# Optimization experiments

Hardware: AMD Instinct MI355X
Metric: run time of the kernel (lower is better)

## Reference

```python
import jax, jax.numpy as jnp
import numpy as np
from jax import lax

C = 128; HEADS = 16; HD = 8; EPS = 1e-5

def _conv3x3(x, w):
    return lax.conv_general_dilated(x, w, (1, 1), 'SAME', dimension_numbers=('NCHW', 'OIHW', 'NCHW'))

def _cbr3(x, w, g, b):
    # Conv3x3 + BatchNorm(eval, running stats folded -> per-channel affine) + ReLU
    return jax.nn.relu(_conv3x3(x, w) * g[:, None, None] + b[:, None, None])

def _cbr1(x, w, g, b):
    y = jnp.einsum('bchw,oc->bohw', x, w)
    return jax.nn.relu(y * g[:, None, None] + b[:, None, None])

def _ln(t, g, b):
    mu = t.mean(-1, keepdims=True)
    va = ((t - mu) ** 2).mean(-1, keepdims=True)
    return (t - mu) / jnp.sqrt(va + EPS) * g + b

def _gconv1x1(xf, w, b, groups):
    # grouped 1x1 conv on flattened spatial dim: xf [B,Cin,N], w [Cout, Cin//groups]
    B, Cin, N = xf.shape
    Cout = w.shape[0]
    y = jnp.einsum('bgcn,goc->bgon', xf.reshape(B, groups, Cin // groups, N),
                   w.reshape(groups, Cout // groups, Cin // groups))
    return y.reshape(B, Cout, N) + b[:, None]

def _ss_softmax(a):
    # sign * sqrt(|a| + 1e-5) then softmax (GISSA's custom transform)
    a = jnp.sign(a) * jnp.sqrt(jnp.abs(a) + 1e-5)
    return jax.nn.softmax(a, axis=-1)

def _gissa(ximg, qkv_w, qkv_b, g, b, qkv2_w, qkv2_b):
    B, Cc, H, W = ximg.shape
    N = H * W
    xf = ximg.reshape(B, Cc, N)
    qkv = _gconv1x1(xf, qkv_w, qkv_b, HEADS).reshape(B, 3, HEADS, HD, N)
    q, k, v = qkv[:, 0], qkv[:, 1], qkv[:, 2]
    attn = _ss_softmax(jnp.einsum('bhdn,bhen->bhde', q, k) * HD ** -0.5)  # [B,h,hd,hd]
    x1 = jnp.einsum('bhde,bhen->bhdn', attn, v).reshape(B, Cc, N) + xf
    x1 = x1.reshape(B, HEADS, HD, N).transpose(0, 2, 1, 3).reshape(B, Cc, N)  # channel shuffle
    y = x1 * g[:, None] + b[:, None]  # BatchNorm eval affine
    xr = jax.nn.relu(y)
    qkv2 = _gconv1x1(xr, qkv2_w, qkv2_b, HD).reshape(B, 3, HD, HEADS, N)
    q2, k2, v2 = qkv2[:, 0], qkv2[:, 1], qkv2[:, 2]
    attn2 = _ss_softmax(jnp.einsum('bdhn,bdgn->bdhg', q2, k2) * HEADS ** -0.5)  # [B,hd,h,h]
    o = jnp.einsum('bdhg,bdgn->bdhn', attn2, v2).transpose(0, 2, 1, 3).reshape(B, Cc, N) + y
    return o.reshape(B, Cc, H, W)

def _swsa_calc(ximg, pi_w, pi_b, g, b, po_w, po_b):
    B, Cc, H, W = ximg.shape
    t = jnp.einsum('bcn,oc->bon', ximg.reshape(B, Cc, H * W), pi_w) + pi_b[:, None]
    t = t * g[:, None] + b[:, None]  # BN affine
    q = t[:, :Cc].transpose(0, 2, 1)  # [B,N,C]
    v = t[:, Cc:].transpose(0, 2, 1)
    atn = jax.nn.softmax(jnp.einsum('bnc,bmc->bnm', q, q) * Cc ** -0.5, axis=-1)
    y = jnp.einsum('bnm,bmc->bnc', atn, v).transpose(0, 2, 1)  # [B,C,N]
    y = (jnp.einsum('bcn,oc->bon', y, po_w) + po_b[:, None]).reshape(B, Cc, H, W)
    return y, atn

def _swsa_reuse(ximg, atn, pi_w, pi_b, g, b, po_w, po_b):
    B, Cc, H, W = ximg.shape
    t = jnp.einsum('bcn,oc->bon', ximg.reshape(B, Cc, H * W), pi_w) + pi_b[:, None]
    t = t * g[:, None] + b[:, None]
    v = t.transpose(0, 2, 1)
    y = (jnp.einsum('bnm,bmc->bnc', atn, v) * Cc ** -0.5).transpose(0, 2, 1)
    return (jnp.einsum('bcn,oc->bon', y, po_w) + po_b[:, None]).reshape(B, Cc, H, W)

def _forward(x, ssfe_w, ssfe_g, ssfe_b, cc_w, cc_g, cc_b, ln1_g, ln1_b, qkv_w, qkv_b, gbn_g, gbn_b, qkv2_w, qkv2_b, ln2_g, ln2_b, mlp_w1, mlp_b1, mlp_w2, mlp_b2, cs_w, cs_g, cs_b, lfe0_w, lfe0_g, lfe0_b, s0_pi_w, s0_pi_b, s0_bn_g, s0_bn_b, s0_po_w, s0_po_b, lfe1_w, lfe1_g, lfe1_b, s1_pi_w, s1_pi_b, s1_bn_g, s1_bn_b, s1_po_w, s1_po_b, lamuda, fc_w):
    B, Cin, H, W = x.shape
    N = H * W
    # SSFE stem (approximated as Conv3x3+BN+ReLU; source def unavailable)
    xs = _cbr3(x, ssfe_w, ssfe_g, ssfe_b)
    # channel branch: 1x1 CBR + SIT (LN -> GISSA -> residual -> LN -> MLP -> residual)
    xc = _cbr1(xs, cc_w, cc_g, cc_b)
    t = xc.reshape(B, C, N).transpose(0, 2, 1)  # [B,N,C]
    cur = _ln(t, ln1_g, ln1_b).transpose(0, 2, 1).reshape(B, C, H, W)
    t = t + _gissa(cur, qkv_w, qkv_b, gbn_g, gbn_b, qkv2_w, qkv2_b).reshape(B, C, N).transpose(0, 2, 1)
    h = _ln(t, ln2_g, ln2_b)
    h = jax.nn.gelu(h @ mlp_w1.T + mlp_b1, approximate=False) @ mlp_w2.T + mlp_b2
    t = t + h
    xc = t.transpose(0, 2, 1).reshape(B, C, H, W)
    # spatial branch: 3x3 CBR + SCA (LFE + SWSA with attention reuse)
    xp = _cbr3(xs, cs_w, cs_g, cs_b)
    xp = _cbr3(xp, lfe0_w, lfe0_g, lfe0_b) + xp
    y, atn = _swsa_calc(xp, s0_pi_w, s0_pi_b, s0_bn_g, s0_bn_b, s0_po_w, s0_po_b)
    xp = y + xp
    xp = _cbr3(xp, lfe1_w, lfe1_g, lfe1_b) + xp
    xp = _swsa_reuse(xp, atn, s1_pi_w, s1_pi_b, s1_bn_g, s1_bn_b, s1_po_w, s1_po_b) + xp
    lmd = jax.nn.sigmoid(lamuda[0])
    out = lmd * xc + (1.0 - lmd) * xp
    return out.mean(axis=(2, 3)) @ fc_w.T  # global avg pool + fc (dropout p=0 for HUST2013)

def setup_inputs():
    ks = iter(jax.random.split(jax.random.key(0), 64))
    def rn(shape, scale=0.05):
        return jax.random.normal(next(ks), shape, jnp.float32) * scale
    ones = lambda *s: jnp.ones(s, jnp.float32)
    zeros = lambda *s: jnp.zeros(s, jnp.float32)
    return dict(
        x=jax.random.normal(next(ks), (32, 144, 32, 32), jnp.float32),
        ssfe_w=rn((144, 144, 3, 3)), ssfe_g=ones(144), ssfe_b=zeros(144),
        cc_w=rn((128, 144)), cc_g=ones(128), cc_b=zeros(128),
        ln1_g=ones(128), ln1_b=zeros(128),
        qkv_w=rn((384, 8)), qkv_b=zeros(384),
        gbn_g=ones(128), gbn_b=zeros(128),
        qkv2_w=rn((384, 16)), qkv2_b=zeros(384),
        ln2_g=ones(128), ln2_b=zeros(128),
        mlp_w1=rn((512, 128)), mlp_b1=zeros(512),
        mlp_w2=rn((128, 512)), mlp_b2=zeros(128),
        cs_w=rn((128, 144, 3, 3)), cs_g=ones(128), cs_b=zeros(128),
        lfe0_w=rn((128, 128, 3, 3)), lfe0_g=ones(128), lfe0_b=zeros(128),
        s0_pi_w=rn((256, 128)), s0_pi_b=zeros(256), s0_bn_g=ones(256), s0_bn_b=zeros(256),
        s0_po_w=rn((128, 128)), s0_po_b=zeros(128),
        lfe1_w=rn((128, 128, 3, 3)), lfe1_g=ones(128), lfe1_b=zeros(128),
        s1_pi_w=rn((128, 128)), s1_pi_b=zeros(128), s1_bn_g=ones(128), s1_bn_b=zeros(128),
        s1_po_w=rn((128, 128)), s1_po_b=zeros(128),
        lamuda=jnp.full((1,), 0.5, jnp.float32),
        fc_w=rn((16, 128)),
    )

def reference(x, ssfe_w, ssfe_g, ssfe_b, cc_w, cc_g, cc_b, ln1_g, ln1_b, qkv_w, qkv_b, gbn_g, gbn_b, qkv2_w, qkv2_b, ln2_g, ln2_b, mlp_w1, mlp_b1, mlp_w2, mlp_b2, cs_w, cs_g, cs_b, lfe0_w, lfe0_g, lfe0_b, s0_pi_w, s0_pi_b, s0_bn_g, s0_bn_b, s0_po_w, s0_po_b, lfe1_w, lfe1_g, lfe1_b, s1_pi_w, s1_pi_b, s1_bn_g, s1_bn_b, s1_po_w, s1_po_b, lamuda, fc_w):
    return _forward(x, ssfe_w, ssfe_g, ssfe_b, cc_w, cc_g, cc_b, ln1_g, ln1_b, qkv_w, qkv_b, gbn_g, gbn_b, qkv2_w, qkv2_b, ln2_g, ln2_b, mlp_w1, mlp_b1, mlp_w2, mlp_b2, cs_w, cs_g, cs_b, lfe0_w, lfe0_g, lfe0_b, s0_pi_w, s0_pi_b, s0_bn_g, s0_bn_b, s0_po_w, s0_po_b, lfe1_w, lfe1_g, lfe1_b, s1_pi_w, s1_pi_b, s1_bn_g, s1_bn_b, s1_po_w, s1_po_b, lamuda, fc_w)
```

## Files before the change

kernel.cpp:

```cpp
#include <hip/hip_runtime.h>
#include <math.h>


static constexpr int NPIX = 1024;

typedef __attribute__((ext_vector_type(8))) short bf16x8;
typedef __attribute__((ext_vector_type(4))) float f32x4;
typedef __attribute__((ext_vector_type(8))) unsigned short u16x8;
typedef __attribute__((ext_vector_type(4))) unsigned short u16x4;

static __device__ __forceinline__ unsigned short f2bf(float f) {
    unsigned u = __builtin_bit_cast(unsigned, f);
    unsigned r = (u + 0x7fffu + ((u >> 16) & 1u)) >> 16;
    return (unsigned short)r;
}
static __device__ __forceinline__ float bf2f(unsigned short u) {
    unsigned v = ((unsigned)u) << 16;
    return __builtin_bit_cast(float, v);
}

__global__ __launch_bounds__(256) void prepack_convs(
    const float* __restrict__ ssfe_w, const float* __restrict__ cs_w,
    const float* __restrict__ lfe0_w, const float* __restrict__ lfe1_w,
    unsigned short* __restrict__ wssfe, unsigned short* __restrict__ wcs,
// ... 41 lines not shown
    } else if (idx < 102400) {
        v = po1_w[idx - 86016];
    } else if (idx < 167936) {
        v = w1[idx - 102400];
    } else {
        v = w2[idx - 167936];
    }
    o[idx] = f2bf(v);
}

__global__ __launch_bounds__(256) void cvt_xT_kernel(
    const float* __restrict__ x, unsigned short* __restrict__ xT0)
{
    __shared__ unsigned short T[64 * 168];
    const int tid = threadIdx.x;
    const int b = blockIdx.x;
    const int px0 = blockIdx.y << 6;
    const float* xb = x + ((size_t)b * 144 << 10) + px0;

#pragma unroll 1
    for (int idx = tid; idx < 72 * 64; idx += 256) {
        const int c2 = idx >> 6, px = idx & 63;
        float a = xb[((size_t)(2 * c2) << 10) + px];
        float c = xb[((size_t)(2 * c2 + 1) << 10) + px];
        *(unsigned*)&T[px * 168 + 2 * c2] =
            (unsigned)f2bf(a) | ((unsigned)f2bf(c) << 16);
    }
#pragma unroll 1
    for (int idx = tid; idx < 64 * 8; idx += 256) {
        const int px = idx >> 3, pr = idx & 7;
        *(unsigned*)&T[px * 168 + 144 + pr * 2] = 0u;
    }
    __syncthreads();

#pragma unroll 1
    for (int idx = tid; idx < 64 * 20; idx += 256) {
        const int px = idx / 20;
        const int chunk = idx - px * 20;
        *(u16x8*)(xT0 + ((size_t)((b << 10) + px0 + px)) * 160 + chunk * 8) =
            *(const u16x8*)&T[px * 168 + chunk * 8];
    }
}

__global__ __launch_bounds__(256) void conv3x3_ssfe_kernel(
    const unsigned short* __restrict__ xT,
    const unsigned short* __restrict__ wrep,
    const float* __restrict__ g, const float* __restrict__ bb,
    unsigned short* __restrict__ outT)
{
    constexpr int CINP = 160, PITCH = 168, NCHK = 20;
    __shared__ unsigned short X[130 * PITCH];
    const int tid = threadIdx.x;
    const int b = blockIdx.x, gr = blockIdx.y;
    const int pbase = gr << 6;
    const int gbase = pbase - 33;
    const int wid = tid >> 6, lane = tid & 63;
    const int ll = lane & 15, lq = lane >> 4;
    const unsigned short* xb = xT + ((size_t)b << 10) * CINP;

#pragma unroll 1
    for (int idx = tid; idx < 130 * NCHK; idx += 256) {
        const int row = idx / NCHK;
        const int chunk = idx - row * NCHK;
        const int gp = gbase + row;
        u16x8 v = {};
        if (gp >= 0 && gp < 1024)
            v = *(const u16x8*)(xb + (size_t)gp * CINP + chunk * 8);
        *(u16x8*)&X[row * PITCH + chunk * 8] = v;
    }
    __syncthreads();

    if (wid == 3) {
#pragma unroll
        for (int j = 0; j < 4; ++j) {
            const int px = pbase + j * 16 + ll;
            u16x4 z = {};
            *(u16x4*)(outT + ((size_t)((b << 10) + px)) * 160 + 144 + lq * 4) = z;
        }
        return;
    }

    const int co0w = wid * 48;
    f32x4 acc[3][4];
#pragma unroll
    for (int i = 0; i < 3; ++i)
#pragma unroll
        for (int j = 0; j < 4; ++j)
#pragma unroll
            for (int r = 0; r < 4; ++r) acc[i][j][r] = 0.f;

#pragma unroll
    for (int tap = 0; tap < 9; ++tap) {
        const int soff = (tap / 3) * 32 + (tap % 3);
        const int dx = tap % 3;
#pragma unroll
        for (int kc = 0; kc < CINP / 32; ++kc) {
            bf16x8 bfv[4];
#pragma unroll
            for (int j = 0; j < 4; ++j) {
                const int p = j * 16 + ll;
                bf16x8 v = *(const bf16x8*)&X[(p + soff) * PITCH + kc * 32 + lq * 8];
                const bool zed = (dx == 0 && (j & 1) == 0 && ll == 0) ||
                                 (dx == 2 && (j & 1) == 1 && ll == 15);
                if (zed) { bf16x8 z = {}; v = z; }
                bfv[j] = v;
            }
            const unsigned short* wb =
                wrep + ((size_t)tap * 144 + co0w) * CINP + kc * 32 + lq * 8;
#pragma unroll
            for (int i = 0; i < 3; ++i) {
                bf16x8 af = *(const bf16x8*)(wb + (size_t)(i * 16 + ll) * CINP);
#pragma unroll
                for (int j = 0; j < 4; ++j)
                    acc[i][j] = __builtin_amdgcn_mfma_f32_16x16x32_bf16(
                        af, bfv[j], acc[i][j], 0, 0, 0);
            }
        }
    }

#pragma unroll
    for (int i = 0; i < 3; ++i) {
        const int cob = co0w + i * 16 + lq * 4;
        float gv[4], bv[4];
#pragma unroll
        for (int r = 0; r < 4; ++r) { gv[r] = g[cob + r]; bv[r] = bb[cob + r]; }
#pragma unroll
        for (int j = 0; j < 4; ++j) {
            const int px = pbase + j * 16 + ll;
            u16x4 tp;
#pragma unroll
            for (int r = 0; r < 4; ++r)
                tp[r] = f2bf(fmaxf(acc[i][j][r] * gv[r] + bv[r], 0.f));
            *(u16x4*)(outT + ((size_t)((b << 10) + px)) * 160 + cob) = tp;
        }
    }
}

template <int CINP>
__global__ __launch_bounds__(256) void conv3x3_lds_kernel(
    const unsigned short* __restrict__ xT,
    const unsigned short* __restrict__ wrep,
    const float* __restrict__ g, const float* __restrict__ bb,
    const unsigned short* __restrict__ resT,
    unsigned short* __restrict__ outT, int Cout)
{
    constexpr int PITCH = CINP + 8;
    constexpr int NCHK = CINP / 8;
    __shared__ unsigned short X[130 * PITCH];
    const int tid = threadIdx.x;
    const int b = blockIdx.x, gr = blockIdx.y;
    const int pbase = gr << 6;
    const int gbase = pbase - 33;
    const int wid = tid >> 6, lane = tid & 63;
    const int ll = lane & 15, lq = lane >> 4;
    const int co0w = wid << 5;
    const unsigned short* xb = xT + ((size_t)b << 10) * CINP;

#pragma unroll 1
    for (int idx = tid; idx < 130 * NCHK; idx += 256) {
        const int row = idx / NCHK;
        const int chunk = idx - row * NCHK;
        const int gp = gbase + row;
        u16x8 v = {};
        if (gp >= 0 && gp < 1024)
            v = *(const u16x8*)(xb + (size_t)gp * CINP + chunk * 8);
        *(u16x8*)&X[row * PITCH + chunk * 8] = v;
    }
    __syncthreads();

    f32x4 acc[2][4];
#pragma unroll
    for (int i = 0; i < 2; ++i)
#pragma unroll
        for (int j = 0; j < 4; ++j)
#pragma unroll
            for (int r = 0; r < 4; ++r) acc[i][j][r] = 0.f;

#pragma unroll
    for (int tap = 0; tap < 9; ++tap) {
        const int soff = (tap / 3) * 32 + (tap % 3);
        const int dx = tap % 3;
#pragma unroll
        for (int kc = 0; kc < CINP / 32; ++kc) {
            bf16x8 bfv[4];
#pragma unroll
            for (int j = 0; j < 4; ++j) {
                const int p = j * 16 + ll;
                bf16x8 v = *(const bf16x8*)&X[(p + soff) * PITCH + kc * 32 + lq * 8];
                const bool zed = (dx == 0 && (j & 1) == 0 && ll == 0) ||
                                 (dx == 2 && (j & 1) == 1 && ll == 15);
                if (zed) { bf16x8 z = {}; v = z; }
                bfv[j] = v;
            }
            const unsigned short* wb =
                wrep + ((size_t)tap * Cout + co0w) * CINP + kc * 32 + lq * 8;
#pragma unroll
            for (int i = 0; i < 2; ++i) {
                bf16x8 af = *(const bf16x8*)(wb + (size_t)(i * 16 + ll) * CINP);
#pragma unroll
                for (int j = 0; j < 4; ++j)
                    acc[i][j] = __builtin_amdgcn_mfma_f32_16x16x32_bf16(
                        af, bfv[j], acc[i][j], 0, 0, 0);
            }
        }
    }

#pragma unroll
    for (int i = 0; i < 2; ++i) {
        const int cob = co0w + i * 16 + lq * 4;
        float gv[4], bv[4];
#pragma unroll
        for (int r = 0; r < 4; ++r) { gv[r] = g[cob + r]; bv[r] = bb[cob + r]; }
#pragma unroll
        for (int j = 0; j < 4; ++j) {
            const int px = pbase + j * 16 + ll;
            const size_t rowT = ((size_t)((b << 10) + px)) << 7;
            u16x4 rv = {};
            if (resT) rv = *(const u16x4*)(resT + rowT + cob);
            u16x4 tp;
#pragma unroll
            for (int r = 0; r < 4; ++r) {
                float v = fmaxf(acc[i][j][r] * gv[r] + bv[r], 0.f);
                if (resT) v += bf2f(rv[r]);
                tp[r] = f2bf(v);
            }
            *(u16x4*)(outT + rowT + cob) = tp;
        }
    }
}

template <int KP>
__global__ __launch_bounds__(256) void lin_mfma_kernel(
    const unsigned short* __restrict__ xT, const unsigned short* __restrict__ wbf,
    const float* __restrict__ bias0, const float* __restrict__ g,
    const float* __restrict__ bb, const unsigned short* __restrict__ resT,
    float* __restrict__ outF, unsigned short* __restrict__ outBF,
    unsigned short* __restrict__ outT, int do_relu)
{
    const int tid = threadIdx.x;
    const int b = blockIdx.x;
    const int n0 = blockIdx.y << 6;
    const int wid = tid >> 6, lane = tid & 63;
    const int ll = lane & 15, lq = lane >> 4;
    const unsigned short* xb = xT + (size_t)((b << 10) + n0) * KP;

    f32x4 acc[2][4];
#pragma unroll
    for (int i = 0; i < 2; ++i)
#pragma unroll
        for (int j = 0; j < 4; ++j)
#pragma unroll
            for (int r = 0; r < 4; ++r) acc[i][j][r] = 0.f;

#pragma unroll
    for (int kk = 0; kk < KP / 32; ++kk) {
        bf16x8 af[2], bfv[4];
#pragma unroll
        for (int i = 0; i < 2; ++i)
            af[i] = *(const bf16x8*)(wbf + (size_t)(wid * 32 + i * 16 + ll) * KP + kk * 32 + lq * 8);
#pragma unroll
        for (int j = 0; j < 4; ++j)
            bfv[j] = *(const bf16x8*)(xb + (size_t)(j * 16 + ll) * KP + kk * 32 + lq * 8);
#pragma unroll
        for (int i = 0; i < 2; ++i)
#pragma unroll
            for (int j = 0; j < 4; ++j)
                acc[i][j] = __builtin_amdgcn_mfma_f32_16x16x32_bf16(af[i], bfv[j], acc[i][j], 0, 0, 0);
    }

#pragma unroll
    for (int i = 0; i < 2; ++i) {
        const int cob = wid * 32 + i * 16 + lq * 4;
        float b0v[4], gv[4], bv[4];
#pragma unroll
        for (int r = 0; r < 4; ++r) {
            b0v[r] = bias0 ? bias0[cob + r] : 0.f;
            gv[r] = g ? g[cob + r] : 1.f;
            bv[r] = g ? bb[cob + r] : 0.f;
        }
#pragma unroll
        for (int j = 0; j < 4; ++j) {
            const int px = n0 + j * 16 + ll;
            const size_t rowT = ((size_t)((b << 10) + px)) << 7;
            u16x4 rv = {};
            if (resT) rv = *(const u16x4*)(resT + rowT + cob);
            u16x4 tp;
#pragma unroll
            for (int r = 0; r < 4; ++r) {
                const int co = cob + r;
                float v = acc[i][j][r] + b0v[r];
                v = v * gv[r] + bv[r];
                if (do_relu) v = fmaxf(v, 0.f);
                if (resT) v += bf2f(rv[r]);
                if (outF) outF[((size_t)((b << 7) + co) << 10) + px] = v;
                unsigned short h = f2bf(v);
                if (outBF) outBF[((size_t)((b << 7) + co) << 10) + px] = h;
                tp[r] = h;
            }
            if (outT) *(u16x4*)(outT + rowT + cob) = tp;
        }
    }
}

__global__ __launch_bounds__(256) void ln_kernel(
    const float* __restrict__ in, const float* __restrict__ g,
    const float* __restrict__ bb, unsigned short* __restrict__ out_bf,
    unsigned short* __restrict__ outT)
{
    const int tid = threadIdx.x;
    const int b = blockIdx.x >> 2;
    const int n = ((blockIdx.x & 3) << 8) + tid;
    const float* ib = in + ((size_t)b << 17) + n;
    float s = 0.f, sq = 0.f;
#pragma unroll 8
    for (int c = 0; c < 128; ++c) {
        float v = ib[(size_t)c << 10];
        s += v;
        sq += v * v;
    }
    const float mu = s * 0.0078125f;
    const float r = rsqrtf(sq * 0.0078125f - mu * mu + 1e-5f);
    unsigned short* obf = out_bf + ((size_t)b << 17) + n;
    unsigned short* oT = outT + (((size_t)b << 10) + n) * 128;
#pragma unroll 2
    for (int c0 = 0; c0 < 128; c0 += 8) {
        u16x8 pk;
#pragma unroll
        for (int e = 0; e < 8; ++e) {
            const int c = c0 + e;
            float v = ib[(size_t)c << 10];
            float y = (v - mu) * r * g[c] + bb[c];
            unsigned short h = f2bf(y);
            obf[(size_t)c << 10] = h;
            pk[e] = h;
        }
        *(u16x8*)(oT + c0) = pk;
    }
}

__global__ __launch_bounds__(256) void gram_kernel(
    const unsigned short* __restrict__ Xbf, float* __restrict__ G)
{
    __shared__ unsigned short Xs[128 * 128];
    const int tid = threadIdx.x;
    const int b = blockIdx.x >> 2;
    const int rg = blockIdx.x & 3;
    const int wid = tid >> 6, lane = tid & 63;
    const int lq = lane >> 4, ll = lane & 15;
    const unsigned short* Xb = Xbf + ((size_t)b << 17);

    f32x4 acc[2][2];
#pragma unroll
    for (int mi = 0; mi < 2; ++mi)
#pragma unroll
        for (int ci = 0; ci < 2; ++ci)
#pragma unroll
            for (int r = 0; r < 4; ++r) acc[mi][ci][r] = 0.f;

#pragma unroll 1
    for (int nt = 0; nt < 8; ++nt) {
        const int n0 = nt << 7;
#pragma unroll
        for (int p = 0; p < 8; ++p) {
            const int ch = (p << 4) + (tid >> 4);
            const int seg = (tid & 15) << 3;
            *(u16x8*)&Xs[ch * 128 + (seg ^ ((ch & 7) << 3))] =
                *(const u16x8*)(Xb + ((size_t)ch << 10) + n0 + seg);
        }
        __syncthreads();
#pragma unroll
        for (int ks = 0; ks < 4; ++ks) {
            bf16x8 af[2], bf_[2];
#pragma unroll
            for (int mi = 0; mi < 2; ++mi) {
                const int ar = (rg << 5) + mi * 16 + ll;
                af[mi] = *(const bf16x8*)&Xs[ar * 128 + ((ks * 32 + lq * 8) ^ ((ar & 7) << 3))];
            }
#pragma unroll
            for (int ci = 0; ci < 2; ++ci) {
                const int br = (wid << 5) + ci * 16 + ll;
                bf_[ci] = *(const bf16x8*)&Xs[br * 128 + ((ks * 32 + lq * 8) ^ ((br & 7) << 3))];
            }
#pragma unroll
            for (int mi = 0; mi < 2; ++mi)
#pragma unroll
                for (int ci = 0; ci < 2; ++ci)
                    acc[mi][ci] = __builtin_amdgcn_mfma_f32_16x16x32_bf16(
                        af[mi], bf_[ci], acc[mi][ci], 0, 0, 0);
        }
        __syncthreads();
    }
    float* Gb = G + ((size_t)b << 14);
#pragma unroll
    for (int mi = 0; mi < 2; ++mi)
#pragma unroll
        for (int ci = 0; ci < 2; ++ci)
#pragma unroll
            for (int r = 0; r < 4; ++r) {
                const int row = (rg << 5) + mi * 16 + lq * 4 + r;
                const int col = (wid << 5) + ci * 16 + ll;
                Gb[row * 128 + col] = acc[mi][ci][r];
            }
}

__global__ __launch_bounds__(256) void sums_kernel(
    const unsigned short* __restrict__ Xbf, float* __restrict__ S)
{
    const int tid = threadIdx.x;
    const int b = blockIdx.x;
    const int ch = tid >> 1, half = tid & 1;
    const unsigned short* p = Xbf + ((size_t)b << 17) + ((size_t)ch << 10) + half * 512;
    float s = 0.f;
#pragma unroll 4
    for (int i = 0; i < 64; ++i) {
        u16x8 v = *(const u16x8*)(p + i * 8);
#pragma unroll
        for (int e = 0; e < 8; ++e) s += bf2f(v[e]);
    }
    s += __shfl_xor(s, 1);
    if (half == 0) S[(b << 7) + ch] = s;
}

__global__ __launch_bounds__(64) void mats1_kernel(
    const float* __restrict__ G, const float* __restrict__ S,
    const float* __restrict__ qkv_w, const float* __restrict__ qkv_b,
    const float* __restrict__ g, const float* __restrict__ bb,
    unsigned short* __restrict__ M1, float* __restrict__ c1)
{
    const int lane = threadIdx.x;
    const int b = blockIdx.x >> 4, h = blockIdx.x & 15;
    const float* Gb = G + ((size_t)b << 14);
    const float* Sb = S + (b << 7);
    const int d = lane >> 3, e = lane & 7;
    const int qch = h * 8 + d, kch = 128 + h * 8 + e;
    const int qoff = (qch / 24) * 8, koff = (kch / 24) * 8;
    float wq[8], wk[8];
#pragma unroll
    for (int i = 0; i < 8; ++i) {
        wq[i] = qkv_w[qch * 8 + i];
        wk[i] = qkv_w[kch * 8 + i];
    }
    float s = 0.f;
#pragma unroll
    for (int i = 0; i < 8; ++i) {
        float gu = 0.f;
#pragma unroll
        for (int j = 0; j < 8; ++j) gu += Gb[(qoff + i) * 128 + koff + j] * wk[j];
        s += wq[i] * gu;
    }
    const float bq = qkv_b[qch], bk = qkv_b[kch];
    float swk = 0.f, swq = 0.f;
#pragma unroll
    for (int j = 0; j < 8; ++j) { swk += wk[j] * Sb[koff + j]; swq += wq[j] * Sb[qoff + j]; }
    s += bq * swk + bk * swq + 1024.f * bq * bk;
    s *= 0.35355339059327373f;
    float a = (s > 0.f) ? sqrtf(s + 1e-5f) : ((s < 0.f) ? -sqrtf(1e-5f - s) : 0.f);
    float mx = a;
    mx = fmaxf(mx, __shfl_xor(mx, 1));
    mx = fmaxf(mx, __shfl_xor(mx, 2));
    mx = fmaxf(mx, __shfl_xor(mx, 4));
    float p = __expf(a - mx);
    float den = p;
    den += __shfl_xor(den, 1);
    den += __shfl_xor(den, 2);
    den += __shfl_xor(den, 4);
    const float A = p / den;

    const int l = e;
    const int cp = d * 16 + h;
    float row[16];
#pragma unroll
    for (int j = 0; j < 16; ++j) row[j] = 0.f;
    float cacc = 0.f;
#pragma unroll
    for (int e2 = 0; e2 < 8; ++e2) {
        const float Ae = __shfl(A, d * 8 + e2);
        const int vch = 256 + h * 8 + e2;
        const int voff = (vch / 24) * 8;
        cacc += Ae * qkv_b[vch];
        if ((voff >> 4) == l) {
            const int base = voff & 15;
#pragma unroll
            for (int j = 0; j < 8; ++j) row[base + j] += Ae * qkv_w[vch * 8 + j];
        }
    }
    const int idc = h * 8 + d;
    if ((idc >> 4) == l) row[idc & 15] += 1.f;
    const float gg = g[cp];
    unsigned short* mrow = M1 + ((size_t)b << 14) + cp * 128 + l * 16;
#pragma unroll
    for (int j = 0; j < 16; ++j) mrow[j] = f2bf(gg * row[j]);
    if (l == 0) c1[(b << 7) + cp] = gg * cacc + bb[cp];
}

__global__ __launch_bounds__(256) void mats2_kernel(
    const float* __restrict__ G, const float* __restrict__ S,
    const float* __restrict__ qkv2_w, const float* __restrict__ qkv2_b,
    unsigned short* __restrict__ M2, float* __restrict__ c2)
{
    const int tid = threadIdx.x;
    const int b = blockIdx.x >> 3, d = blockIdx.x & 7;
    const float* Gb = G + ((size_t)b << 14);
    const float* Sb = S + (b << 7);
    const int h = tid >> 4, gq = tid & 15;
    const int q2ch = d * 16 + h, k2ch = 128 + d * 16 + gq;
    const int qoff = (q2ch / 48) * 16, koff = (k2ch / 48) * 16;
    float wq[16], wk[16];
#pragma unroll
    for (int i = 0; i < 16; ++i) {
        wq[i] = qkv2_w[q2ch * 16 + i];
        wk[i] = qkv2_w[k2ch * 16 + i];
    }
    float s = 0.f;
#pragma unroll
    for (int i = 0; i < 16; ++i) {
        float gu = 0.f;
#pragma unroll
        for (int j = 0; j < 16; ++j) gu += Gb[(qoff + i) * 128 + koff + j] * wk[j];
        s += wq[i] * gu;
    }
    const float bq = qkv2_b[q2ch], bk = qkv2_b[k2ch];
    float swk = 0.f, swq = 0.f;
#pragma unroll
    for (int j = 0; j < 16; ++j) { swk += wk[j] * Sb[koff + j]; swq += wq[j] * Sb[qoff + j]; }
    s += bq * swk + bk * swq + 1024.f * bq * bk;
    s *= 0.25f;
    float a = (s > 0.f) ? sqrtf(s + 1e-5f) : ((s < 0.f) ? -sqrtf(1e-5f - s) : 0.f);
    float mx = a;
    mx = fmaxf(mx, __shfl_xor(mx, 1));
    mx = fmaxf(mx, __shfl_xor(mx, 2));
    mx = fmaxf(mx, __shfl_xor(mx, 4));
    mx = fmaxf(mx, __shfl_xor(mx, 8));
    float p = __expf(a - mx);
    float den = p;
    den += __shfl_xor(den, 1);
    den += __shfl_xor(den, 2);
    den += __shfl_xor(den, 4);
    den += __shfl_xor(den, 8);
    const float A2 = p / den;

    const int l = gq;
    float row[8];
#pragma unroll
    for (int j = 0; j < 8; ++j) row[j] = 0.f;
    float cacc = 0.f;
#pragma unroll
    for (int g2 = 0; g2 < 16; ++g2) {
        const float Ag = __shfl(A2, (tid & 48) + g2);
        const int v2ch = 256 + d * 16 + g2;
        const int voff = (v2ch / 48) * 16;
        cacc += Ag * qkv2_b[v2ch];
        if ((l >> 1) == (voff >> 4)) {
            const int base = (l & 1) * 8;
#pragma unroll
            for (int j = 0; j < 8; ++j) row[j] += Ag * qkv2_w[v2ch * 16 + base + j];
        }
    }
    const int c = h * 8 + d;
    unsigned short* mrow = M2 + ((size_t)b << 14) + c * 128 + l * 8;
#pragma unroll
    for (int j = 0; j < 8; ++j) mrow[j] = f2bf(row[j]);
    if (l == 0) c2[(b << 7) + c] = cacc;
}

__global__ __launch_bounds__(256) void apply1_mfma_kernel(
    const unsigned short* __restrict__ curT, const unsigned short* __restrict__ M1bf,
    const float* __restrict__ c1, float* __restrict__ ybuf,
    unsigned short* __restrict__ yrbf, unsigned short* __restrict__ yrT)
{
    const int tid = threadIdx.x;
    const int b = blockIdx.x >> 3;
    const int n0 = (blockIdx.x & 7) << 7;
    const int wid = tid >> 6, lane = tid & 63;
    const int wr = wid >> 1, wc = wid & 1;
    const int ll = lane & 15, lq = lane >> 4;
    const unsigned short* Mb = M1bf + ((size_t)b << 14);
    const unsigned short* xb = curT + (((size_t)b << 10) + n0 + wc * 64) * 128;

    f32x4 acc[4][4];
#pragma unroll
    for (int i = 0; i < 4; ++i)
#pragma unroll
        for (int j = 0; j < 4; ++j)
#pragma unroll
            for (int r = 0; r < 4; ++r) acc[i][j][r] = 0.f;

#pragma unroll
    for (int kk = 0; kk < 4; ++kk) {
        bf16x8 af[4], bfv[4];
#pragma unroll
        for (int i = 0; i < 4; ++i)
            af[i] = *(const bf16x8*)(Mb + (size_t)(wr * 64 + i * 16 + ll) * 128 + kk * 32 + lq * 8);
#pragma unroll
        for (int j = 0; j < 4; ++j)
            bfv[j] = *(const bf16x8*)(xb + (size_t)(j * 16 + ll) * 128 + kk * 32 + lq * 8);
#pragma unroll
        for (int i = 0; i < 4; ++i)
#pragma unroll
            for (int j = 0; j < 4; ++j)
                acc[i][j] = __builtin_amdgcn_mfma_f32_16x16x32_bf16(af[i], bfv[j], acc[i][j], 0, 0, 0);
    }

#pragma unroll
    for (int i = 0; i < 4; ++i) {
        const int cob = wr * 64 + i * 16 + lq * 4;
        float c1v[4];
#pragma unroll
        for (int r = 0; r < 4; ++r) c1v[r] = c1[(b << 7) + cob + r];
#pragma unroll
        for (int j = 0; j < 4; ++j) {
            const int px = n0 + wc * 64 + j * 16 + ll;
            u16x4 tp;
#pragma unroll
            for (int r = 0; r < 4; ++r) {
                const int co = cob + r;
                const float v = acc[i][j][r] + c1v[r];
                const size_t oi = ((size_t)(b * 128 + co) << 10) + px;
                ybuf[oi] = v;
                const unsigned short h = f2bf(fmaxf(v, 0.f));
                yrbf[oi] = h;
                tp[r] = h;
            }
            *(u16x4*)(yrT + (((size_t)b << 10) + px) * 128 + cob) = tp;
        }
    }
}

__global__ __launch_bounds__(256) void apply2_mfma_kernel(
    const unsigned short* __restrict__ yrT, const unsigned short* __restrict__ M2bf,
    const float* __restrict__ c2, const float* __restrict__ ybuf,
    float* __restrict__ t)
{
    const int tid = threadIdx.x;
    const int b = blockIdx.x >> 3;
    const int n0 = (blockIdx.x & 7) << 7;
    const int wid = tid >> 6, lane = tid & 63;
    const int wr = wid >> 1, wc = wid & 1;
    const int ll = lane & 15, lq = lane >> 4;
    const unsigned short* Mb = M2bf + ((size_t)b << 14);
    const unsigned short* xb = yrT + (((size_t)b << 10) + n0 + wc * 64) * 128;

    f32x4 acc[4][4];
#pragma unroll
    for (int i = 0; i < 4; ++i)
#pragma unroll
        for (int j = 0; j < 4; ++j)
#pragma unroll
            for (int r = 0; r < 4; ++r) acc[i][j][r] = 0.f;

#pragma unroll
    for (int kk = 0; kk < 4; ++kk) {
        bf16x8 af[4], bfv[4];
#pragma unroll
        for (int i = 0; i < 4; ++i)
            af[i] = *(const bf16x8*)(Mb + (size_t)(wr * 64 + i * 16 + ll) * 128 + kk * 32 + lq * 8);
#pragma unroll
        for (int j = 0; j < 4; ++j)
            bfv[j] = *(const bf16x8*)(xb + (size_t)(j * 16 + ll) * 128 + kk * 32 + lq * 8);
#pragma unroll
        for (int i = 0; i < 4; ++i)
#pragma unroll
            for (int j = 0; j < 4; ++j)
                acc[i][j] = __builtin_amdgcn_mfma_f32_16x16x32_bf16(af[i], bfv[j], acc[i][j], 0, 0, 0);
    }

#pragma unroll
    for (int i = 0; i < 4; ++i) {
        const int cob = wr * 64 + i * 16 + lq * 4;
        float c2v[4];
#pragma unroll
        for (int r = 0; r < 4; ++r) c2v[r] = c2[(b << 7) + cob + r];
#pragma unroll
        for (int j = 0; j < 4; ++j) {
            const int px = n0 + wc * 64 + j * 16 + ll;
#pragma unroll
            for (int r = 0; r < 4; ++r) {
                const size_t oi = ((size_t)(b * 128 + cob + r) << 10) + px;
                t[oi] += acc[i][j][r] + c2v[r] + ybuf[oi];
            }
        }
    }
}

__global__ __launch_bounds__(256) void mlp_mfma_kernel(
    float* __restrict__ t, const float* __restrict__ ln_g,
    const float* __restrict__ ln_b, const unsigned short* __restrict__ w1bf,
    const float* __restrict__ b1, const unsigned short* __restrict__ w2bf,
    const float* __restrict__ b2)
{
    __shared__ unsigned char lds[16384 + 65536];
    unsigned char* xnb = lds;
    unsigned char* hb = lds + 16384;

    const int tid = threadIdx.x;
    const int b = blockIdx.x >> 4;
    const int n0 = (blockIdx.x & 15) << 6;
    float* tb = t + ((size_t)b << 17) + n0;

    {
        const int px = tid >> 2, q = tid & 3;
        float v[32];
        float s = 0.f, sq = 0.f;
#pragma unroll
        for (int k = 0; k < 32; ++k) {
            float x = tb[((size_t)(q * 32 + k) << 10) + px];
            v[k] = x;
            s += x;
            sq += x * x;
        }
        s += __shfl_xor(s, 1); s += __shfl_xor(s, 2);
        sq += __shfl_xor(sq, 1); sq += __shfl_xor(sq, 2);
        const float mu = s * 0.0078125f;
        const float rstd = rsqrtf(sq * 0.0078125f - mu * mu + 1e-5f);
        const int sw = (px & 7) << 4;
#pragma unroll
        for (int cc = 0; cc < 4; ++cc) {
            u16x8 pk;
#pragma unroll
            for (int e = 0; e < 8; ++e) {
                int c = q * 32 + cc * 8 + e;
                float xv = (v[cc * 8 + e] - mu) * rstd * ln_g[c] + ln_b[c];
                pk[e] = f2bf(xv);
            }
            *(u16x8*)(xnb + px * 256 + ((q * 64 + cc * 16) ^ sw)) = pk;
        }
    }
    __syncthreads();

    const int wid = tid >> 6, lane = tid & 63;
    const int lr = lane & 15, lk = lane >> 4;

#pragma unroll 1
    for (int pass = 0; pass < 2; ++pass) {
        const int hidbase = (wid << 7) + (pass << 6);
        f32x4 acc[4][4];
#pragma unroll
        for (int i = 0; i < 4; ++i)
#pragma unroll
            for (int j = 0; j < 4; ++j)
#pragma unroll
                for (int r = 0; r < 4; ++r) acc[i][j][r] = 0.f;
#pragma unroll
        for (int kk = 0; kk < 4; ++kk) {
            bf16x8 af[4], bfr[4];
#pragma unroll
            for (int i = 0; i < 4; ++i)
                af[i] = *(const bf16x8*)(w1bf + (size_t)(hidbase + i * 16 + lr) * 128 + kk * 32 + lk * 8);
#pragma unroll
            for (int j = 0; j < 4; ++j) {
                const int px = j * 16 + lr;
                bfr[j] = *(const bf16x8*)(xnb + px * 256 + ((kk * 64 + lk * 16) ^ ((px & 7) << 4)));
            }
#pragma unroll
            for (int i = 0; i < 4; ++i)
#pragma unroll
                for (int j = 0; j < 4; ++j)
                    acc[i][j] = __builtin_amdgcn_mfma_f32_16x16x32_bf16(af[i], bfr[j], acc[i][j], 0, 0, 0);
        }
#pragma unroll
        for (int i = 0; i < 4; ++i) {
            const int hid0 = hidbase + i * 16 + lk * 4;
            float bi[4];
#pragma unroll
            for (int r = 0; r < 4; ++r) bi[r] = b1[hid0 + r];
#pragma unroll
            for (int j = 0; j < 4; ++j) {
                const int px = j * 16 + lr;
                u16x4 pk;
#pragma unroll
                for (int r = 0; r < 4; ++r) {
                    float x = acc[i][j][r] + bi[r];
                    float u = 1.5957691f * x * (1.f + 0.044715f * x * x);
                    float gv = x / (1.f + __expf(-u));
                    pk[r] = f2bf(gv);
                }
                *(u16x4*)(hb + px * 1024 + ((hid0 * 2) ^ ((px & 7) << 4))) = pk;
            }
        }
    }
    __syncthreads();

    f32x4 acc2[2][4];
#pragma unroll
    for (int i = 0; i < 2; ++i)
#pragma unroll
        for (int j = 0; j < 4; ++j)
#pragma unroll
            for (int r = 0; r < 4; ++r) acc2[i][j][r] = 0.f;
#pragma unroll 2
    for (int ks = 0; ks < 16; ++ks) {
        bf16x8 af[2], bfr[4];
#pragma unroll
        for (int i = 0; i < 2; ++i)
            af[i] = *(const bf16x8*)(w2bf + (size_t)((wid << 5) + i * 16 + lr) * 512 + ks * 32 + lk * 8);
#pragma unroll
        for (int j = 0; j < 4; ++j) {
            const int px = j * 16 + lr;
            bfr[j] = *(const bf16x8*)(hb + px * 1024 + ((ks * 64 + lk * 16) ^ ((px & 7) << 4)));
        }
#pragma unroll
        for (int i = 0; i < 2; ++i)
#pragma unroll
            for (int j = 0; j < 4; ++j)
                acc2[i][j] = __builtin_amdgcn_mfma_f32_16x16x32_bf16(af[i], bfr[j], acc2[i][j], 0, 0, 0);
    }
#pragma unroll
    for (int i = 0; i < 2; ++i) {
        const int cb = (wid << 5) + i * 16 + lk * 4;
        float b2v[4];
#pragma unroll
        for (int r = 0; r < 4; ++r) b2v[r] = b2[cb + r];
#pragma unroll
        for (int j = 0; j < 4; ++j) {
            const int px = j * 16 + lr;
#pragma unroll
            for (int r = 0; r < 4; ++r) {
                const size_t off = ((size_t)(cb + r) << 10) + px;
                tb[off] += acc2[i][j][r] + b2v[r];
            }
        }
    }
}

__global__ __launch_bounds__(256) void swsa_mfma_kernel(
    const unsigned short* __restrict__ qT, const unsigned short* __restrict__ vbf,
    unsigned short* __restrict__ outT, float fscale)
{
    __shared__ unsigned short K_lds[128 * 128];
    __shared__ unsigned short V_lds[128 * 128];
    const int tid = threadIdx.x;
    const int b = blockIdx.x & 31;
    const int n0 = (blockIdx.x >> 5) << 6;
    const int wid = tid >> 6, lane = tid & 63;
    const int lq = lane >> 4, ll = lane & 15;
    const unsigned short* qTb = qT + ((size_t)b << 17);
    const unsigned short* vb = vbf + ((size_t)b << 17);

    bf16x8 aq[4];
    {
        const int row = n0 + wid * 16 + ll;
#pragma unroll
        for (int kk = 0; kk < 4; ++kk)
            aq[kk] = *(const bf16x8*)(qTb + ((size_t)row << 7) + kk * 32 + lq * 8);
    }

    float mrun[4], lrun[4];
#pragma unroll
    for (int i = 0; i < 4; ++i) { mrun[i] = -INFINITY; lrun[i] = 0.f; }
    f32x4 yacc[8];
#pragma unroll
    for (int cj = 0; cj < 8; ++cj)
#pragma unroll
        for (int r = 0; r < 4; ++r) yacc[cj][r] = 0.f;

#pragma unroll 1
    for (int mt = 0; mt < 8; ++mt) {
        const int m0 = mt << 7;
        for (int ch = tid; ch < 2048; ch += 256) {
            const int rr = ch >> 4, e0 = (ch & 15) << 3;
            const int sw = (rr & 7) << 3;
            *(u16x8*)&K_lds[rr * 128 + (e0 ^ sw)] =
                *(const u16x8*)(qTb + ((size_t)(m0 + rr) << 7) + e0);
            *(u16x8*)&V_lds[rr * 128 + (e0 ^ sw)] =
                *(const u16x8*)(vb + ((size_t)rr << 10) + m0 + e0);
        }
        __syncthreads();

        f32x4 sacc[8];
#pragma unroll
        for (int j = 0; j < 8; ++j)
#pragma unroll
            for (int r = 0; r < 4; ++r) sacc[j][r] = 0.f;
#pragma unroll
        for (int j = 0; j < 8; ++j) {
            const int ml = j * 16 + ll;
            const int swk = (ml & 7) << 3;
#pragma unroll
            for (int kk = 0; kk < 4; ++kk) {
                bf16x8 bk = *(const bf16x8*)&K_lds[ml * 128 + ((kk * 32 + lq * 8) ^ swk)];
                sacc[j] = __builtin_amdgcn_mfma_f32_16x16x32_bf16(aq[kk], bk, sacc[j], 0, 0, 0);
            }
        }
        __syncthreads();

        float pmax[4];
#pragma unroll
        for (int i = 0; i < 4; ++i) pmax[i] = -INFINITY;
#pragma unroll
        for (int j = 0; j < 8; ++j)
#pragma unroll
            for (int r = 0; r < 4; ++r) {
                float s = sacc[j][r] * 0.08838834764831845f;
                sacc[j][r] = s;
                pmax[r] = fmaxf(pmax[r], s);
            }
        float alpha[4];
#pragma unroll
        for (int i = 0; i < 4; ++i) {
            float m = pmax[i];
            m = fmaxf(m, __shfl_xor(m, 1));
            m = fmaxf(m, __shfl_xor(m, 2));
            m = fmaxf(m, __shfl_xor(m, 4));
            m = fmaxf(m, __shfl_xor(m, 8));
            const float mn = fmaxf(mrun[i], m);
            alpha[i] = __expf(mrun[i] - mn);
            mrun[i] = mn;
        }
        float psum[4];
#pragma unroll
        for (int r = 0; r < 4; ++r) {
            const int nbw = wid * 16 + lq * 4 + r;
            const int sw4 = ((nbw >> 2) & 3) << 4;
            const float mn = mrun[r];
            float ps = 0.f;
#pragma unroll
            for (int j = 0; j < 8; ++j) {
                float p = __expf(sacc[j][r] - mn);
                ps += p;
                K_lds[nbw * 128 + ((j * 16 + ll) ^ sw4)] = f2bf(p);
            }
            psum[r] = ps;
        }
#pragma unroll
        for (int i = 0; i < 4; ++i) {
            float s = psum[i];
            s += __shfl_xor(s, 1);
            s += __shfl_xor(s, 2);
            s += __shfl_xor(s, 4);
            s += __shfl_xor(s, 8);
            lrun[i] = lrun[i] * alpha[i] + s;
        }
#pragma unroll
        for (int cj = 0; cj < 8; ++cj)
#pragma unroll
            for (int r = 0; r < 4; ++r) yacc[cj][r] *= alpha[r];

        bf16x8 ap[4];
        {
            const int nb = wid * 16 + ll;
            const int sw4 = ((nb >> 2) & 3) << 4;
#pragma unroll
            for (int mk = 0; mk < 4; ++mk)
                ap[mk] = *(const bf16x8*)&K_lds[nb * 128 + ((mk * 32 + lq * 8) ^ sw4)];
        }
#pragma unroll
        for (int cj = 0; cj < 8; ++cj) {
            const int cl = cj * 16 + ll;
            const int sw = (cl & 7) << 3;
#pragma unroll
            for (int mk = 0; mk < 4; ++mk) {
                bf16x8 bv = *(const bf16x8*)&V_lds[cl * 128 + ((mk * 32 + lq * 8) ^ sw)];
                yacc[cj] = __builtin_amdgcn_mfma_f32_16x16x32_bf16(ap[mk], bv, yacc[cj], 0, 0, 0);
            }
        }
        __syncthreads();
    }

    const int nbase = n0 + wid * 16 + lq * 4;
    float inv[4];
#pragma unroll
    for (int r = 0; r < 4; ++r) inv[r] = fscale / lrun[r];
#pragma unroll
    for (int cj = 0; cj < 8; ++cj) {
        const int c = cj * 16 + ll;
        unsigned short* tb = outT + ((size_t)((b << 10) + nbase)) * 128 + c;
        tb[0]   = f2bf(yacc[cj][0] * inv[0]);
        tb[128] = f2bf(yacc[cj][1] * inv[1]);
        tb[256] = f2bf(yacc[cj][2] * inv[2]);
        tb[384] = f2bf(yacc[cj][3] * inv[3]);
    }
}

__global__ __launch_bounds__(256) void mean_kernel(
    const float* __restrict__ xc, const float* __restrict__ xp,
    const float* __restrict__ lamuda, float* __restrict__ meanb)
{
    const int wid = threadIdx.x >> 6, lane = threadIdx.x & 63;
    const int row = (blockIdx.x << 2) + wid;
    const float lmd = 1.f / (1.f + __expf(-lamuda[0]));
    const float* a = xc + ((size_t)row << 10) + (lane << 2);
    const float* d = xp + ((size_t)row << 10) + (lane << 2);
    float s = 0.f;
#pragma unroll
    for (int i = 0; i < 4; ++i) {
        float4 va = *(const float4*)(a + (i << 8));
        float4 vd = *(const float4*)(d + (i << 8));
        s += lmd * (va.x + va.y + va.z + va.w) +
             (1.f - lmd) * (vd.x + vd.y + vd.z + vd.w);
    }
#pragma unroll
    for (int o = 1; o < 64; o <<= 1) s += __shfl_xor(s, o);
    if (lane == 0) meanb[row] = s * (1.f / 1024.f);
}

__global__ __launch_bounds__(256) void fc_kernel(
    const float* __restrict__ meanb, const float* __restrict__ fc_w,
    float* __restrict__ outp)
{
    const int idx = blockIdx.x * 256 + threadIdx.x;
    if (idx >= 512) return;
    const int b = idx >> 4, o = idx & 15;
    float s = 0.f;
#pragma unroll 4
    for (int c = 0; c < 128; ++c) s += fc_w[o * 128 + c] * meanb[b * 128 + c];
    outp[b * 16 + o] = s;
}

extern "C" void kernel_launch(void* const* d_in, const int* in_sizes, int n_in,
                              void* d_out, int out_size, void* d_ws, size_t ws_size,
                              hipStream_t stream)
{
    (void)in_sizes; (void)n_in; (void)out_size; (void)ws_size;

    const float* x       = (const float*)d_in[0];
    const float* ssfe_w  = (const float*)d_in[1];
    const float* ssfe_g  = (const float*)d_in[2];
    const float* ssfe_b  = (const float*)d_in[3];
    const float* cc_w    = (const float*)d_in[4];
    const float* cc_g    = (const float*)d_in[5];
    const float* cc_b    = (const float*)d_in[6];
    const float* ln1_g   = (const float*)d_in[7];
    const float* ln1_b   = (const float*)d_in[8];
    const float* qkv_w   = (const float*)d_in[9];
    const float* qkv_b   = (const float*)d_in[10];
    const float* gbn_g   = (const float*)d_in[11];
    const float* gbn_b   = (const float*)d_in[12];
    const float* qkv2_w  = (const float*)d_in[13];
    const float* qkv2_b  = (const float*)d_in[14];
    const float* ln2_g   = (const float*)d_in[15];
    const float* ln2_b   = (const float*)d_in[16];
    const float* mlp_w1  = (const float*)d_in[17];
    const float* mlp_b1  = (const float*)d_in[18];
    const float* mlp_w2  = (const float*)d_in[19];
    const float* mlp_b2  = (const float*)d_in[20];
    const float* cs_w    = (const float*)d_in[21];
    const float* cs_g    = (const float*)d_in[22];
    const float* cs_b    = (const float*)d_in[23];
    const float* lfe0_w  = (const float*)d_in[24];
    const float* lfe0_g  = (const float*)d_in[25];
    const float* lfe0_b  = (const float*)d_in[26];
    const float* s0_pi_w = (const float*)d_in[27];
    const float* s0_pi_b = (const float*)d_in[28];
    const float* s0_bn_g = (const float*)d_in[29];
    const float* s0_bn_b = (const float*)d_in[30];
    const float* s0_po_w = (const float*)d_in[31];
    const float* s0_po_b = (const float*)d_in[32];
    const float* lfe1_w  = (const float*)d_in[33];
    const float* lfe1_g  = (const float*)d_in[34];
    const float* lfe1_b  = (const float*)d_in[35];
    const float* s1_pi_w = (const float*)d_in[36];
    const float* s1_pi_b = (const float*)d_in[37];
    const float* s1_bn_g = (const float*)d_in[38];
    const float* s1_bn_b = (const float*)d_in[39];
    const float* s1_po_w = (const float*)d_in[40];
    const float* s1_po_b = (const float*)d_in[41];
    const float* lamuda  = (const float*)d_in[42];
    const float* fc_w    = (const float*)d_in[43];
    float* out = (float*)d_out;
    float* ws = (float*)d_ws;

    float* xs = ws;
    float* t  = ws + 4718592;
    float* Qr = ws + 13107200;
    float* P2 = ws + 25690112;
    float* P3 = ws + 29884416;

    unsigned short* xT0 = (unsigned short*)Qr;

    unsigned short* curbf = (unsigned short*)Qr;
    unsigned short* curT  = (unsigned short*)(Qr + 2097152);
    unsigned short* yrbf  = (unsigned short*)(Qr + 4194304);
    unsigned short* yrT   = (unsigned short*)(Qr + 6291456);
    unsigned short* xsT   = (unsigned short*)(Qr + 8388608);
    float* ybuf = P2;

    unsigned short* xpT   = (unsigned short*)Qr;
    unsigned short* qT0   = (unsigned short*)Qr;
    unsigned short* v0    = (unsigned short*)(Qr + 2097152);
    unsigned short* yvT   = (unsigned short*)(Qr + 4194304);
    unsigned short* v1    = (unsigned short*)(Qr + 4194304);
    unsigned short* xp3T  = (unsigned short*)(Qr + 6291456);
    unsigned short* yv2T  = (unsigned short*)(Qr + 6291456);
    unsigned short* xp2T  = (unsigned short*)(Qr + 8388608);
    unsigned short* xp4T  = (unsigned short*)(Qr + 8388608);

    unsigned short* linw  = (unsigned short*)(Qr + 11010048);
    unsigned short* wcc   = linw;
    unsigned short* wpi0  = linw + 20480;
    unsigned short* wpi1  = linw + 53248;
    unsigned short* wpo0  = linw + 69632;
    unsigned short* wpo1  = linw + 86016;
    unsigned short* w1bf  = linw + 102400;
    unsigned short* w2bf  = linw + 167936;
    float* meanb = Qr + 11200000;

    float* Gbuf  = P3 + 1048576;
    float* Sbuf  = P3 + 1572864;
    unsigned short* M1bf = (unsigned short*)(P3 + 1576960);
    float* c1buf = P3 + 1839104;
    unsigned short* M2bf = (unsigned short*)(P3 + 1843200);
    float* c2buf = P3 + 2105344;

    unsigned short* wssfe = (unsigned short*)P3;
    unsigned short* wcs   = (unsigned short*)(P3 + 131072);
    unsigned short* wlfe0 = (unsigned short*)(P3 + 262144);
    unsigned short* wlfe1 = (unsigned short*)xs;

    const dim3 blk(256);

    prepack_convs<<<dim3((686592 + 255) / 256), blk, 0, stream>>>(
        ssfe_w, cs_w, lfe0_w, lfe1_w, wssfe, wcs, wlfe0, wlfe1);
    prepack_lins<<<dim3((233472 + 255) / 256), blk, 0, stream>>>(
        cc_w, s0_pi_w, s1_pi_w, s0_po_w, s1_po_w, mlp_w1, mlp_w2, linw);

    cvt_xT_kernel<<<dim3(32, 16), blk, 0, stream>>>(x, xT0);
    conv3x3_ssfe_kernel<<<dim3(32, 16), blk, 0, stream>>>(
        xT0, wssfe, ssfe_g, ssfe_b, xsT);
    lin_mfma_kernel<160><<<dim3(32, 16), blk, 0, stream>>>(
        xsT, wcc, nullptr, cc_g, cc_b, nullptr, t, nullptr, nullptr, 1);

    ln_kernel<<<dim3(128), blk, 0, stream>>>(t, ln1_g, ln1_b, curbf, curT);
    gram_kernel<<<dim3(128), blk, 0, stream>>>(curbf, Gbuf);
    sums_kernel<<<dim3(32), blk, 0, stream>>>(curbf, Sbuf);
    mats1_kernel<<<dim3(512), dim3(64), 0, stream>>>(Gbuf, Sbuf, qkv_w, qkv_b, gbn_g, gbn_b, M1bf, c1buf);
    apply1_mfma_kernel<<<dim3(256), blk, 0, stream>>>(curT, M1bf, c1buf, ybuf, yrbf, yrT);
    gram_kernel<<<dim3(128), blk, 0, stream>>>(yrbf, Gbuf);
    sums_kernel<<<dim3(32), blk, 0, stream>>>(yrbf, Sbuf);
    mats2_kernel<<<dim3(256), blk, 0, stream>>>(Gbuf, Sbuf, qkv2_w, qkv2_b, M2bf, c2buf);
    apply2_mfma_kernel<<<dim3(256), blk, 0, stream>>>(yrT, M2bf, c2buf, ybuf, t);

    mlp_mfma_kernel<<<dim3(512), blk, 0, stream>>>(t, ln2_g, ln2_b, w1bf, mlp_b1, w2bf, mlp_b2);

    conv3x3_lds_kernel<160><<<dim3(32, 16), blk, 0, stream>>>(
        xsT, wcs, cs_g, cs_b, nullptr, xpT, 128);
    conv3x3_lds_kernel<128><<<dim3(32, 16), blk, 0, stream>>>(
        xpT, wlfe0, lfe0_g, lfe0_b, xpT, xp2T, 128);
    lin_mfma_kernel<128><<<dim3(32, 16), blk, 0, stream>>>(
        xp2T, wpi0, s0_pi_b, s0_bn_g, s0_bn_b, nullptr, nullptr, nullptr, qT0, 0);
    lin_mfma_kernel<128><<<dim3(32, 16), blk, 0, stream>>>(
        xp2T, wpi0 + (size_t)128 * 128, s0_pi_b + 128, s0_bn_g + 128, s0_bn_b + 128,
        nullptr, nullptr, v0, nullptr, 0);
    swsa_mfma_kernel<<<dim3(512), blk, 0, stream>>>(qT0, v0, yvT, 1.0f);
    lin_mfma_kernel<128><<<dim3(32, 16), blk, 0, stream>>>(
        yvT, wpo0, s0_po_b, nullptr, nullptr, xp2T, nullptr, nullptr, xp3T, 0);
    conv3x3_lds_kernel<128><<<dim3(32, 16), blk, 0, stream>>>(
        xp3T, wlfe1, lfe1_g, lfe1_b, xp3T, xp4T, 128);
    lin_mfma_kernel<128><<<dim3(32, 16), blk, 0, stream>>>(
        xp4T, wpi1, s1_pi_b, s1_bn_g, s1_bn_b, nullptr, nullptr, v1, nullptr, 0);
    swsa_mfma_kernel<<<dim3(512), blk, 0, stream>>>(qT0, v1, yv2T, 0.08838834764831845f);
    lin_mfma_kernel<128><<<dim3(32, 16), blk, 0, stream>>>(
        yv2T, wpo1, s1_po_b, nullptr, nullptr, xp4T, P3, nullptr, nullptr, 0);

    mean_kernel<<<dim3(1024), blk, 0, stream>>>(t, P3, lamuda, meanb);
    fc_kernel<<<dim3(2), blk, 0, stream>>>(meanb, fc_w, out);
}
```

Measured before the change: 448.5 us.

## Fuse SWSA output projection into attention kernel and merge q/v input projections

Adds a pi0 kernel that computes both the q and v halves of the first SWSA input projection in one launch instead of two lin_mfma launches. The swsa kernel now stages its normalized attention output in LDS and applies the output projection, bias and residual in place, which removes the separate po lin_mfma launches and their intermediate buffers. This cuts launches and global round trips of the attention output. The cost is heavier per-block epilogues and an extra LDS pass with another barrier.

```diff
diff --git a/kernel.cpp b/kernel.cpp
--- a/kernel.cpp
+++ b/kernel.cpp
@@ -367,6 +367,75 @@
     }
 }
 
+__global__ __launch_bounds__(256) void pi0_kernel(
+    const unsigned short* __restrict__ xT, const unsigned short* __restrict__ wbf,
+    const float* __restrict__ bias0, const float* __restrict__ g,
+    const float* __restrict__ bb, unsigned short* __restrict__ qTout,
+    unsigned short* __restrict__ vout)
+{
+    const int tid = threadIdx.x;
+    const int b = blockIdx.x;
+    const int n0 = blockIdx.y << 6;
+    const int wid = tid >> 6, lane = tid & 63;
+    const int ll = lane & 15, lq = lane >> 4;
+    const int co0 = wid << 6;
+    const unsigned short* xb = xT + (size_t)((b << 10) + n0) * 128;
+
+    f32x4 acc[4][4];
+#pragma unroll
+    for (int i = 0; i < 4; ++i)
+#pragma unroll
+        for (int j = 0; j < 4; ++j)
+#pragma unroll
+            for (int r = 0; r < 4; ++r) acc[i][j][r] = 0.f;
+
+#pragma unroll
+    for (int kk = 0; kk < 4; ++kk) {
+        bf16x8 af[4], bfv[4];
+#pragma unroll
+        for (int i = 0; i < 4; ++i)
+            af[i] = *(const bf16x8*)(wbf + (size_t)(co0 + i * 16 + ll) * 128 + kk * 32 + lq * 8);
+#pragma unroll
+        for (int j = 0; j < 4; ++j)
+            bfv[j] = *(const bf16x8*)(xb + (size_t)(j * 16 + ll) * 128 + kk * 32 + lq * 8);
+#pragma unroll
+        for (int i = 0; i < 4; ++i)
+#pragma unroll
+            for (int j = 0; j < 4; ++j)
+                acc[i][j] = __builtin_amdgcn_mfma_f32_16x16x32_bf16(af[i], bfv[j], acc[i][j], 0, 0, 0);
+    }
+
+#pragma unroll
+    for (int i = 0; i < 4; ++i) {
+        const int cob = co0 + i * 16 + lq * 4;
+        float b0v[4], gv[4], bv[4];
+#pragma unroll
+        for (int r = 0; r < 4; ++r) {
+            b0v[r] = bias0[cob + r];
+            gv[r] = g[cob + r];
+            bv[r] = bb[cob + r];
+        }
+#pragma unroll
+        for (int j = 0; j < 4; ++j) {
+            const int px = n0 + j * 16 + ll;
+            float vv[4];
+#pragma unroll
+            for (int r = 0; r < 4; ++r)
+                vv[r] = (acc[i][j][r] + b0v[r]) * gv[r] + bv[r];
+            if (wid < 2) {
+                u16x4 tp;
+#pragma unroll
+                for (int r = 0; r < 4; ++r) tp[r] = f2bf(vv[r]);
+                *(u16x4*)(qTout + (((size_t)((b << 10) + px)) << 7) + cob) = tp;
+            } else {
+#pragma unroll
+                for (int r = 0; r < 4; ++r)
+                    vout[((size_t)(b * 128 + cob - 128 + r) << 10) + px] = f2bf(vv[r]);
+            }
+        }
+    }
+}
+
 __global__ __launch_bounds__(256) void ln_kernel(
     const float* __restrict__ in, const float* __restrict__ g,
     const float* __restrict__ bb, unsigned short* __restrict__ out_bf,
@@ -887,9 +956,11 @@
     }
 }
 
-__global__ __launch_bounds__(256) void swsa_mfma_kernel(
+__global__ __launch_bounds__(256) void swsa_po_kernel(
     const unsigned short* __restrict__ qT, const unsigned short* __restrict__ vbf,
-    unsigned short* __restrict__ outT, float fscale)
+    const unsigned short* __restrict__ wpo, const float* __restrict__ po_b,
+    const unsigned short* __restrict__ resT,
+    unsigned short* __restrict__ outT, float* __restrict__ outF, float fscale)
 {
     __shared__ unsigned short K_lds[128 * 128];
     __shared__ unsigned short V_lds[128 * 128];
@@ -1021,18 +1092,77 @@
         __syncthreads();
     }
 
-    const int nbase = n0 + wid * 16 + lq * 4;
-    float inv[4];
-#pragma unroll
-    for (int r = 0; r < 4; ++r) inv[r] = fscale / lrun[r];
-#pragma unroll
-    for (int cj = 0; cj < 8; ++cj) {
-        const int c = cj * 16 + ll;
-        unsigned short* tb = outT + ((size_t)((b << 10) + nbase)) * 128 + c;
-        tb[0]   = f2bf(yacc[cj][0] * inv[0]);
-        tb[128] = f2bf(yacc[cj][1] * inv[1]);
-        tb[256] = f2bf(yacc[cj][2] * inv[2]);
-        tb[384] = f2bf(yacc[cj][3] * inv[3]);
+    {
+        float inv[4];
+#pragma unroll
+        for (int r = 0; r < 4; ++r) inv[r] = fscale / lrun[r];
+        const int rw0 = wid * 16 + lq * 4;
+#pragma unroll
+        for (int cj = 0; cj < 8; ++cj) {
+            const int c = cj * 16 + ll;
+#pragma unroll
+            for (int r = 0; r < 4; ++r) {
+                const int row = rw0 + r;
+                const int sw4 = ((row >> 2) & 3) << 4;
+                K_lds[row * 128 + (c ^ sw4)] = f2bf(yacc[cj][r] * inv[r]);
+            }
+        }
+    }
+    __syncthreads();
+
+    f32x4 acc2[2][4];
+#pragma unroll
+    for (int i = 0; i < 2; ++i)
+#pragma unroll
+        for (int j = 0; j < 4; ++j)
+#pragma unroll
+            for (int r = 0; r < 4; ++r) acc2[i][j][r] = 0.f;
+#pragma unroll
+    for (int kk = 0; kk < 4; ++kk) {
+        bf16x8 af[2], bfv[4];
+#pragma unroll
+        for (int i = 0; i < 2; ++i)
+            af[i] = *(const bf16x8*)(wpo + (size_t)(wid * 32 + i * 16 + ll) * 128 + kk * 32 + lq * 8);
+#pragma unroll
+        for (int j = 0; j < 4; ++j) {
+            const int row = j * 16 + ll;
+            const int sw4 = ((row >> 2) & 3) << 4;
+            bfv[j] = *(const bf16x8*)&K_lds[row * 128 + ((kk * 32 + lq * 8) ^ sw4)];
+        }
+#pragma unroll
+        for (int i = 0; i < 2; ++i)
+#pragma unroll
+            for (int j = 0; j < 4; ++j)
+                acc2[i][j] = __builtin_amdgcn_mfma_f32_16x16x32_bf16(af[i], bfv[j], acc2[i][j], 0, 0, 0);
+    }
+
+#pragma unroll
+    for (int i = 0; i < 2; ++i) {
+        const int cob = wid * 32 + i * 16 + lq * 4;
+        float pob[4];
+#pragma unroll
+        for (int r = 0; r < 4; ++r) pob[r] = po_b[cob + r];
+#pragma unroll
+        for (int j = 0; j < 4; ++j) {
+            const int px = n0 + j * 16 + ll;
+            const size_t rowT = ((size_t)((b << 10) + px)) << 7;
+            u16x4 rv = *(const u16x4*)(resT + rowT + cob);
+            float vv[4];
+#pragma unroll
+            for (int r = 0; r < 4; ++r)
+                vv[r] = acc2[i][j][r] + pob[r] + bf2f(rv[r]);
+            if (outT) {
+                u16x4 tp;
+#pragma unroll
+                for (int r = 0; r < 4; ++r) tp[r] = f2bf(vv[r]);
+                *(u16x4*)(outT + rowT + cob) = tp;
+            }
+            if (outF) {
+#pragma unroll
+                for (int r = 0; r < 4; ++r)
+                    outF[((size_t)(b * 128 + cob + r) << 10) + px] = vv[r];
+            }
+        }
     }
 }
 
@@ -1142,10 +1272,8 @@
     unsigned short* xpT   = (unsigned short*)Qr;
     unsigned short* qT0   = (unsigned short*)Qr;
     unsigned short* v0    = (unsigned short*)(Qr + 2097152);
-    unsigned short* yvT   = (unsigned short*)(Qr + 4194304);
     unsigned short* v1    = (unsigned short*)(Qr + 4194304);
     unsigned short* xp3T  = (unsigned short*)(Qr + 6291456);
-    unsigned short* yv2T  = (unsigned short*)(Qr + 6291456);
     unsigned short* xp2T  = (unsigned short*)(Qr + 8388608);
     unsigned short* xp4T  = (unsigned short*)(Qr + 8388608);
 
@@ -1200,21 +1328,16 @@
         xsT, wcs, cs_g, cs_b, nullptr, xpT, 128);
     conv3x3_lds_kernel<128><<<dim3(32, 16), blk, 0, stream>>>(
         xpT, wlfe0, lfe0_g, lfe0_b, xpT, xp2T, 128);
-    lin_mfma_kernel<128><<<dim3(32, 16), blk, 0, stream>>>(
-        xp2T, wpi0, s0_pi_b, s0_bn_g, s0_bn_b, nullptr, nullptr, nullptr, qT0, 0);
-    lin_mfma_kernel<128><<<dim3(32, 16), blk, 0, stream>>>(
-        xp2T, wpi0 + (size_t)128 * 128, s0_pi_b + 128, s0_bn_g + 128, s0_bn_b + 128,
-        nullptr, nullptr, v0, nullptr, 0);
-    swsa_mfma_kernel<<<dim3(512), blk, 0, stream>>>(qT0, v0, yvT, 1.0f);
-    lin_mfma_kernel<128><<<dim3(32, 16), blk, 0, stream>>>(
-        yvT, wpo0, s0_po_b, nullptr, nullptr, xp2T, nullptr, nullptr, xp3T, 0);
+    pi0_kernel<<<dim3(32, 16), blk, 0, stream>>>(
+        xp2T, wpi0, s0_pi_b, s0_bn_g, s0_bn_b, qT0, v0);
+    swsa_po_kernel<<<dim3(512), blk, 0, stream>>>(
+        qT0, v0, wpo0, s0_po_b, xp2T, xp3T, nullptr, 1.0f);
     conv3x3_lds_kernel<128><<<dim3(32, 16), blk, 0, stream>>>(
         xp3T, wlfe1, lfe1_g, lfe1_b, xp3T, xp4T, 128);
     lin_mfma_kernel<128><<<dim3(32, 16), blk, 0, stream>>>(
         xp4T, wpi1, s1_pi_b, s1_bn_g, s1_bn_b, nullptr, nullptr, v1, nullptr, 0);
-    swsa_mfma_kernel<<<dim3(512), blk, 0, stream>>>(qT0, v1, yv2T, 0.08838834764831845f);
-    lin_mfma_kernel<128><<<dim3(32, 16), blk, 0, stream>>>(
-        yv2T, wpo1, s1_po_b, nullptr, nullptr, xp4T, P3, nullptr, nullptr, 0);
+    swsa_po_kernel<<<dim3(512), blk, 0, stream>>>(
+        qT0, v1, wpo1, s1_po_b, xp4T, nullptr, P3, 0.08838834764831845f);
 
     mean_kernel<<<dim3(1024), blk, 0, stream>>>(t, P3, lamuda, meanb);
     fc_kernel<<<dim3(2), blk, 0, stream>>>(meanb, fc_w, out);
```

After: 432.8 us. -3.5%, faster.
